# Performance work log

Hardware: AMD Instinct MI355X
Metric: run time of the kernel (lower is better)

## Reference

```python
import jax, jax.numpy as jnp
import numpy as np
from jax import lax

B, CIN, COUT, H, W = 4, 256, 256, 64, 64
K = 3  # kernel size
PAD = 1
STRIDE = 1


def setup_inputs() -> dict:
    key = jax.random.key(0)
    k1, k2, k3, k4 = jax.random.split(key, 4)
    x = jax.random.normal(k1, (B, CIN, H, W), dtype=jnp.float32)
    # small offset weights so learned offsets are modest (original init is zeros)
    offset_w = jax.random.normal(k2, (3 * K * K, CIN, K, K), dtype=jnp.float32) * 0.01
    offset_b = jax.random.normal(k3, (3 * K * K,), dtype=jnp.float32) * 0.01
    dcn_w = jax.random.normal(k4, (COUT, CIN, K, K), dtype=jnp.float32) * (1.0 / np.sqrt(CIN * K * K))
    return {"x": x, "offset_w": offset_w, "offset_b": offset_b, "dcn_w": dcn_w}


def _dcnv2(x, offset_w, offset_b, dcn_w):
    b, c, h, w = x.shape
    kk = K * K
    # offset conv (standard 3x3, stride 1, pad 1)
    o = lax.conv_general_dilated(
        x, offset_w, (STRIDE, STRIDE), ((PAD, PAD), (PAD, PAD)),
        dimension_numbers=("NCHW", "OIHW", "NCHW"))
    o = o + offset_b[None, :, None, None]
    ho, wo = o.shape[2], o.shape[3]
    off = o[:, : 2 * kk].reshape(b, kk, 2, ho, wo)  # pairs are (dy, dx)
    dy, dx = off[:, :, 0], off[:, :, 1]             # [b,kk,ho,wo]
    mask = jax.nn.sigmoid(o[:, 2 * kk:])            # [b,kk,ho,wo]

    ki, kj = jnp.meshgrid(jnp.arange(K), jnp.arange(K), indexing="ij")
    ki = ki.reshape(kk).astype(jnp.float32)
    kj = kj.reshape(kk).astype(jnp.float32)
    base_y = (jnp.arange(ho, dtype=jnp.float32) * STRIDE - PAD)[None, None, :, None] + ki[None, :, None, None]
    base_x = (jnp.arange(wo, dtype=jnp.float32) * STRIDE - PAD)[None, None, None, :] + kj[None, :, None, None]
    py = base_y + dy  # [b,kk,ho,wo] sampling y
    px = base_x + dx  # sampling x

    y0 = jnp.floor(py)
    x0 = jnp.floor(px)
    wy = py - y0  # bilinear fractional weights
    wx = px - x0
    y0i = y0.astype(jnp.int32)
    x0i = x0.astype(jnp.int32)

    xT = x.transpose(0, 2, 3, 1)  # [b,h,w,c] for channel-last gathers
    bidx = jnp.arange(b)[:, None, None, None]

    def gather(yi, xi):
        # zero padding outside the image
        valid = (yi >= 0) & (yi < h) & (xi >= 0) & (xi < w)
        yc = jnp.clip(yi, 0, h - 1)
        xc = jnp.clip(xi, 0, w - 1)
        v = xT[bidx, yc, xc]  # [b,kk,ho,wo,c]
        return v * valid[..., None].astype(x.dtype)

    g00 = gather(y0i, x0i)
    g01 = gather(y0i, x0i + 1)
    g10 = gather(y0i + 1, x0i)
    g11 = gather(y0i + 1, x0i + 1)

    wy_ = wy[..., None]
    wx_ = wx[..., None]
    sampled = (g00 * (1 - wy_) * (1 - wx_) + g01 * (1 - wy_) * wx_
               + g10 * wy_ * (1 - wx_) + g11 * wy_ * wx_)
    sampled = sampled * mask[..., None]  # modulation

    wk = dcn_w.reshape(dcn_w.shape[0], c, kk)  # [o,c,kk]
    return jnp.einsum("bkhwc,ock->bohw", sampled, wk)


def reference(x, offset_w, offset_b, dcn_w):
    return _dcnv2(x, offset_w, offset_b, dcn_w)
```

## Files before the change

### kernel.cpp

```cpp
#include <hip/hip_runtime.h>
#include <hip/hip_bf16.h>
#include <stdint.h>
#include <math.h>

#define KDIM 2304

typedef __attribute__((ext_vector_type(8))) short bf16x8;
typedef __attribute__((ext_vector_type(8))) unsigned short u16x8;
typedef __attribute__((ext_vector_type(4))) float f32x4;

__device__ inline unsigned short f2bf(float f) {
  union { float f; unsigned int u; } v; v.f = f;
  unsigned int u = v.u;
  unsigned int r = (u + 0x7FFFu + ((u >> 16) & 1u)) >> 16;
  return (unsigned short)r;
}
__device__ inline float bf2f(unsigned short h) {
  union { unsigned int u; float f; } v; v.u = ((unsigned int)h) << 16;
  return v.f;
}

__device__ inline void gl2lds16(const void* g, void* l) {
  __builtin_amdgcn_global_load_lds((const __attribute__((address_space(1))) void*)g,
                                   (__attribute__((address_space(3))) void*)l,
                                   16, 0, 0);
}

__global__ __launch_bounds__(256) void k_transpose(const float* __restrict__ x,
                                                   unsigned short* __restrict__ xTb) {
  __shared__ float tile[32][33];
  int t = threadIdx.x;
  int tx = t & 31, ty = t >> 5;
  int p0 = blockIdx.x * 32;
  int c0 = blockIdx.y * 32;
  int b  = blockIdx.z;
  const float* xb = x + ((size_t)b << 20);
#pragma unroll
  for (int i = 0; i < 4; ++i) {
    int c = c0 + ty + i * 8;
    tile[ty + i * 8][tx] = xb[((size_t)c << 12) + p0 + tx];
  }
  __syncthreads();
  unsigned short* ob = xTb + ((size_t)b << 20);
#pragma unroll
  for (int i = 0; i < 4; ++i) {
    int p = p0 + ty + i * 8;
    ob[(((size_t)p) << 8) + c0 + tx] = f2bf(tile[tx][ty + i * 8]);
  }
}

__global__ __launch_bounds__(256) void k_wprep(const float* __restrict__ dcn_w,
                                               const float* __restrict__ offset_w,
                                               unsigned short* __restrict__ Wpk,
                                               unsigned short* __restrict__ Wob,
                                               unsigned short* __restrict__ zp) {
  int gid = blockIdx.x * 256 + threadIdx.x;
  const int N1 = 72 * 8192;
  const int N2 = 32 * KDIM;
  if (gid < N1) {
    int j = gid & 7;
    int lane = (gid >> 3) & 63;
    int mb = (gid >> 9) & 15;
    int kc = gid >> 13;
    int row = mb * 16 + (lane & 15);
    int gk = kc * 32 + ((lane >> 4) << 3) + j;
    int c = gk & 255, kidx = gk >> 8;
    Wpk[gid] = f2bf(dcn_w[((size_t)(row * 256 + c)) * 9 + kidx]);
  } else if (gid < N1 + N2) {
    int g = gid - N1;
    int ch = g / KDIM, k = g % KDIM;
    int kidx = k >> 8, c = k & 255;
    Wob[g] = (ch < 27) ? f2bf(offset_w[((size_t)(ch * 256 + c)) * 9 + kidx])
                       : (unsigned short)0;
  } else if (gid < N1 + N2 + 128) {
    zp[gid - N1 - N2] = 0;
  }
}

__global__ __launch_bounds__(256) void k_offs_gemm(const unsigned short* __restrict__ xTb,
                                                   const unsigned short* __restrict__ Wob,
                                                   const unsigned short* __restrict__ zp,
                                                   const float* __restrict__ offb,
                                                   float* __restrict__ O2) {
  __shared__ unsigned short As[64 * 32];
  __shared__ unsigned short Bs[32 * 32];
  int t = threadIdx.x;
  int wv = t >> 6, lane = t & 63;
  int n0 = blockIdx.x * 64;
  int r0 = t >> 2, coff = (t & 3) * 8;

  int rowA = n0 + r0;
  int b_ = rowA >> 12, hw = rowA & 4095, h = hw >> 6, w = hw & 63;

  f32x4 acc[2] = {};
  char* AsB = (char*)As;
  char* BsB = (char*)Bs;

  for (int kt = 0; kt < 72; ++kt) {
    int k0 = kt * 32;
    int kidx = k0 >> 8, c0 = k0 & 255;
    int di = kidx / 3 - 1, dj = kidx % 3 - 1;
    {
      int y = h + di, xx = w + dj;
      const unsigned short* g = (y >= 0 && y < 64 && xx >= 0 && xx < 64)
          ? xTb + (((((size_t)b_) << 12) + (y << 6) + xx) << 8) + c0 + coff
          : zp;
      gl2lds16(g, AsB + wv * 1024);
    }
    if (t < 128) {
      const unsigned short* g = Wob + (size_t)(t >> 2) * KDIM + k0 + coff;
      gl2lds16(g, BsB + wv * 1024);
    }
    __syncthreads();
    bf16x8 aF, bF[2];
    aF = *(const bf16x8*)(As + (wv * 16 + (lane & 15)) * 32 + (lane >> 4) * 8);
#pragma unroll
    for (int j = 0; j < 2; ++j)
      bF[j] = *(const bf16x8*)(Bs + (j * 16 + (lane & 15)) * 32 + (lane >> 4) * 8);
#pragma unroll
    for (int j = 0; j < 2; ++j)
      acc[j] = __builtin_amdgcn_mfma_f32_16x16x32_bf16(aF, bF[j], acc[j], 0, 0, 0);
    __syncthreads();
  }

  int quad = lane >> 4, cl = lane & 15;
#pragma unroll
  for (int j = 0; j < 2; ++j) {
    int col = j * 16 + cl;
    float bias = (col < 27) ? offb[col] : 0.f;
#pragma unroll
    for (int r = 0; r < 4; ++r) {
      int row = n0 + wv * 16 + quad * 4 + r;
      O2[(size_t)row * 32 + col] = acc[j][r] + bias;
    }
  }
}

__global__ __launch_bounds__(256) void k_sweights(const float* __restrict__ O2,
                                                  float* __restrict__ SW) {
  int gid = blockIdx.x * 256 + threadIdx.x;
  if (gid >= 9 * 16384) return;
  int k = gid >> 14;
  int bhw = gid & 16383;
  int h = (bhw >> 6) & 63, w = bhw & 63;

  const float* o = O2 + (size_t)bhw * 32;
  float dy = o[2 * k];
  float dx = o[2 * k + 1];
  float mv = o[18 + k];
  float mask = 1.0f / (1.0f + expf(-mv));

  float py = (float)(h - 1 + k / 3) + dy;
  float px = (float)(w - 1 + k % 3) + dx;
  float y0f = floorf(py), x0f = floorf(px);
  float wy = py - y0f, wx = px - x0f;
  int y0 = (int)y0f, x0 = (int)x0f;
  int y1 = y0 + 1, x1 = x0 + 1;

  float vy0 = (y0 >= 0 && y0 < 64) ? 1.f : 0.f;
  float vy1 = (y1 >= 0 && y1 < 64) ? 1.f : 0.f;
  float vx0 = (x0 >= 0 && x0 < 64) ? 1.f : 0.f;
  float vx1 = (x1 >= 0 && x1 < 64) ? 1.f : 0.f;
  int y0c = min(max(y0, 0), 63), y1c = min(max(y1, 0), 63);
  int x0c = min(max(x0, 0), 63), x1c = min(max(x1, 0), 63);

  float4 wv4;
  wv4.x = (1.f - wy) * (1.f - wx) * vy0 * vx0 * mask;
  wv4.y = (1.f - wy) * wx * vy0 * vx1 * mask;
  wv4.z = wy * (1.f - wx) * vy1 * vx0 * mask;
  wv4.w = wy * wx * vy1 * vx1 * mask;
  uint4 ov;
  ov.x = (unsigned)(((y0c << 6) + x0c) << 8);
  ov.y = (unsigned)(((y0c << 6) + x1c) << 8);
  ov.z = (unsigned)(((y1c << 6) + x0c) << 8);
  ov.w = (unsigned)(((y1c << 6) + x1c) << 8);

  float* p = SW + (size_t)gid * 8;
  *(float4*)p = wv4;
  *(uint4*)(p + 4) = ov;
}

__global__ __launch_bounds__(256) void k_fused(const unsigned short* __restrict__ Wpk,
                                               const unsigned short* __restrict__ xTb,
                                               const float* __restrict__ SW,
                                               float* __restrict__ out) {
  __shared__ __align__(16) unsigned short Bs[2][64 * 40];
  int t = threadIdx.x;
  int wv = t >> 6, lane = t & 63;
  int n0 = blockIdx.x * 64;
  int b  = n0 >> 12;
  const unsigned short* xb = xTb + ((size_t)b << 20);

  int r = t >> 2, g = t & 3;
  int ch0 = g * 8;
  int bsw = r * 40 + ch0;

  const unsigned short* wpBase = Wpk + ((size_t)(wv * 4 * 64 + lane)) * 8;

  f32x4 acc[4][4] = {};

  float4 wv4; uint4 ov;
  {
    const float* sw = SW + ((size_t)(n0 + r)) * 8;
    wv4 = *(const float4*)sw;
    ov  = *(const uint4*)(sw + 4);
  }
  u16x8 q00, q01, q10, q11;
  bf16x8 aF[4], aFn[4];

  {
    int c = ch0;
    q00 = *(const u16x8*)(xb + ov.x + c);
    q01 = *(const u16x8*)(xb + ov.y + c);
    q10 = *(const u16x8*)(xb + ov.z + c);
    q11 = *(const u16x8*)(xb + ov.w + c);
#pragma unroll
    for (int i = 0; i < 4; ++i)
      aF[i] = *(const bf16x8*)(wpBase + (size_t)i * 512);
  }

#pragma unroll 2
  for (int kt = 0; kt < 72; ++kt) {
    float s[8];
#pragma unroll
    for (int c = 0; c < 8; ++c)
      s[c] = wv4.x * bf2f(q00[c]) + wv4.y * bf2f(q01[c])
           + wv4.z * bf2f(q10[c]) + wv4.w * bf2f(q11[c]);
    union { __hip_bfloat162 h2[4]; bf16x8 v; } pk;
#pragma unroll
    for (int c = 0; c < 4; ++c)
      pk.h2[c] = __float22bfloat162_rn(make_float2(s[2 * c], s[2 * c + 1]));
    *(bf16x8*)(&Bs[kt & 1][bsw]) = pk.v;

    if (kt < 71) {
      int kn = kt + 1;
      if ((kn & 7) == 0) {
        const float* sw = SW + ((size_t)(((kn >> 3) << 14) + n0 + r)) * 8;
        wv4 = *(const float4*)sw;
        ov  = *(const uint4*)(sw + 4);
      }
      int c = ((kn & 7) << 5) + ch0;
      q00 = *(const u16x8*)(xb + ov.x + c);
      q01 = *(const u16x8*)(xb + ov.y + c);
      q10 = *(const u16x8*)(xb + ov.z + c);
      q11 = *(const u16x8*)(xb + ov.w + c);
#pragma unroll
      for (int i = 0; i < 4; ++i)
        aFn[i] = *(const bf16x8*)(wpBase + ((size_t)kn * 16 + i) * 512);
    }

    __syncthreads();
    bf16x8 bF[4];
#pragma unroll
    for (int j = 0; j < 4; ++j)
      bF[j] = *(const bf16x8*)(&Bs[kt & 1][(j * 16 + (lane & 15)) * 40 + (lane >> 4) * 8]);
#pragma unroll
    for (int i = 0; i < 4; ++i)
#pragma unroll
      for (int j = 0; j < 4; ++j)
        acc[i][j] = __builtin_amdgcn_mfma_f32_16x16x32_bf16(aF[i], bF[j], acc[i][j], 0, 0, 0);
    if (kt < 71) {
#pragma unroll
      for (int i = 0; i < 4; ++i) aF[i] = aFn[i];
    }
  }

  int quad = lane >> 4, cl = lane & 15;
  float* ob = out + (((size_t)b) << 20);
#pragma unroll
  for (int i = 0; i < 4; ++i) {
    int mbase = wv * 64 + i * 16 + quad * 4;
#pragma unroll
    for (int j = 0; j < 4; ++j) {
      int hw = (n0 & 4095) + j * 16 + cl;
      float* op = ob + hw;
#pragma unroll
      for (int rr = 0; rr < 4; ++rr)
        op[((size_t)(mbase + rr)) << 12] = acc[i][j][rr];
    }
  }
}

extern "C" void kernel_launch(void* const* d_in, const int* in_sizes, int n_in,
                              void* d_out, int out_size, void* d_ws, size_t ws_size,
                              hipStream_t stream) {
  const float* x        = (const float*)d_in[0];
  const float* offset_w = (const float*)d_in[1];
  const float* offset_b = (const float*)d_in[2];
  const float* dcn_w    = (const float*)d_in[3];
  float* out = (float*)d_out;

  char* ws = (char*)d_ws;
  size_t off = 0;
  auto carve = [&](size_t bytes) -> void* {
    void* p = ws + off;
    off += (bytes + 255) & ~(size_t)255;
    return p;
  };
  unsigned short* xTb = (unsigned short*)carve(4ull * 64 * 64 * 256 * 2);
  unsigned short* Wpk = (unsigned short*)carve(72ull * 8192 * 2);
  unsigned short* Wob = (unsigned short*)carve(32ull * KDIM * 2);
  unsigned short* zp  = (unsigned short*)carve(256);
  float*          O2  = (float*)carve(16384ull * 32 * 4);
  float*          SW  = (float*)carve(9ull * 16384 * 8 * 4);
  (void)ws_size; (void)in_sizes; (void)n_in; (void)out_size;

  k_transpose<<<dim3(128, 8, 4), 256, 0, stream>>>(x, xTb);
  k_wprep<<<dim3((72 * 8192 + 32 * KDIM + 128 + 255) / 256), 256, 0, stream>>>(
      dcn_w, offset_w, Wpk, Wob, zp);
  k_offs_gemm<<<dim3(256), 256, 0, stream>>>(xTb, Wob, zp, offset_b, O2);
  k_sweights<<<dim3((9 * 16384 + 255) / 256), 256, 0, stream>>>(O2, SW);
  k_fused<<<dim3(256), 256, 0, stream>>>(Wpk, xTb, SW, out);
}
```

Baseline: 161.3 us.

## Split offset GEMM over K and widen fused kernel to eight waves

The offset-conv GEMM is split in half along K across a second grid dimension. The two partial results are summed together with the bias inside the sampling-weights kernel, which doubles the number of blocks for that small GEMM. The fused deformable GEMM now uses 512 threads with 8 waves split 4x2 over M and N. Each thread gathers and interpolates 4 channels instead of 8, and each wave holds half as many accumulators. The aim is more parallelism and latency hiding on 256 CUs, at the cost of extra partial-sum traffic and narrower gather loads.

```diff
diff --git a/kernel.cpp b/kernel.cpp
--- a/kernel.cpp
+++ b/kernel.cpp
@@ -6,7 +6,6 @@
 #define KDIM 2304
 
 typedef __attribute__((ext_vector_type(8))) short bf16x8;
-typedef __attribute__((ext_vector_type(8))) unsigned short u16x8;
 typedef __attribute__((ext_vector_type(4))) float f32x4;
 
 __device__ inline unsigned short f2bf(float f) {
@@ -80,13 +79,13 @@
 __global__ __launch_bounds__(256) void k_offs_gemm(const unsigned short* __restrict__ xTb,
                                                    const unsigned short* __restrict__ Wob,
                                                    const unsigned short* __restrict__ zp,
-                                                   const float* __restrict__ offb,
-                                                   float* __restrict__ O2) {
+                                                   float* __restrict__ O2p) {
   __shared__ unsigned short As[64 * 32];
   __shared__ unsigned short Bs[32 * 32];
   int t = threadIdx.x;
   int wv = t >> 6, lane = t & 63;
   int n0 = blockIdx.x * 64;
+  int z = blockIdx.y;
   int r0 = t >> 2, coff = (t & 3) * 8;
 
   int rowA = n0 + r0;
@@ -96,7 +95,7 @@
   char* AsB = (char*)As;
   char* BsB = (char*)Bs;
 
-  for (int kt = 0; kt < 72; ++kt) {
+  for (int kt = z * 36; kt < z * 36 + 36; ++kt) {
     int k0 = kt * 32;
     int kidx = k0 >> 8, c0 = k0 & 255;
     int di = kidx / 3 - 1, dj = kidx % 3 - 1;
@@ -124,19 +123,20 @@
   }
 
   int quad = lane >> 4, cl = lane & 15;
+  float* O2z = O2p + (size_t)z * 16384 * 32;
 #pragma unroll
   for (int j = 0; j < 2; ++j) {
     int col = j * 16 + cl;
-    float bias = (col < 27) ? offb[col] : 0.f;
 #pragma unroll
     for (int r = 0; r < 4; ++r) {
       int row = n0 + wv * 16 + quad * 4 + r;
-      O2[(size_t)row * 32 + col] = acc[j][r] + bias;
-    }
-  }
-}
-
-__global__ __launch_bounds__(256) void k_sweights(const float* __restrict__ O2,
+      O2z[(size_t)row * 32 + col] = acc[j][r];
+    }
+  }
+}
+
+__global__ __launch_bounds__(256) void k_sweights(const float* __restrict__ O2p,
+                                                  const float* __restrict__ offb,
                                                   float* __restrict__ SW) {
   int gid = blockIdx.x * 256 + threadIdx.x;
   if (gid >= 9 * 16384) return;
@@ -144,10 +144,11 @@
   int bhw = gid & 16383;
   int h = (bhw >> 6) & 63, w = bhw & 63;
 
-  const float* o = O2 + (size_t)bhw * 32;
-  float dy = o[2 * k];
-  float dx = o[2 * k + 1];
-  float mv = o[18 + k];
+  const float* o0 = O2p + (size_t)bhw * 32;
+  const float* o1 = o0 + (size_t)16384 * 32;
+  float dy = o0[2 * k]     + o1[2 * k]     + offb[2 * k];
+  float dx = o0[2 * k + 1] + o1[2 * k + 1] + offb[2 * k + 1];
+  float mv = o0[18 + k]    + o1[18 + k]    + offb[18 + k];
   float mask = 1.0f / (1.0f + expf(-mv));
 
   float py = (float)(h - 1 + k / 3) + dy;
@@ -180,24 +181,25 @@
   *(uint4*)(p + 4) = ov;
 }
 
-__global__ __launch_bounds__(256) void k_fused(const unsigned short* __restrict__ Wpk,
+__global__ __launch_bounds__(512) void k_fused(const unsigned short* __restrict__ Wpk,
                                                const unsigned short* __restrict__ xTb,
                                                const float* __restrict__ SW,
                                                float* __restrict__ out) {
   __shared__ __align__(16) unsigned short Bs[2][64 * 40];
   int t = threadIdx.x;
   int wv = t >> 6, lane = t & 63;
+  int wm = wv & 3, wn = wv >> 2;
   int n0 = blockIdx.x * 64;
   int b  = n0 >> 12;
   const unsigned short* xb = xTb + ((size_t)b << 20);
 
-  int r = t >> 2, g = t & 3;
-  int ch0 = g * 8;
+  int r = t >> 3, g = t & 7;
+  int ch0 = g * 4;
   int bsw = r * 40 + ch0;
 
-  const unsigned short* wpBase = Wpk + ((size_t)(wv * 4 * 64 + lane)) * 8;
-
-  f32x4 acc[4][4] = {};
+  const unsigned short* wpBase = Wpk + ((size_t)(wm * 4 * 64 + lane)) * 8;
+
+  f32x4 acc[4][2] = {};
 
   float4 wv4; uint4 ov;
   {
@@ -205,15 +207,15 @@
     wv4 = *(const float4*)sw;
     ov  = *(const uint4*)(sw + 4);
   }
-  u16x8 q00, q01, q10, q11;
+  ushort4 q00, q01, q10, q11;
   bf16x8 aF[4], aFn[4];
 
   {
-    int c = ch0;
-    q00 = *(const u16x8*)(xb + ov.x + c);
-    q01 = *(const u16x8*)(xb + ov.y + c);
-    q10 = *(const u16x8*)(xb + ov.z + c);
-    q11 = *(const u16x8*)(xb + ov.w + c);
+    unsigned c = (unsigned)ch0;
+    q00 = *(const ushort4*)(xb + ov.x + c);
+    q01 = *(const ushort4*)(xb + ov.y + c);
+    q10 = *(const ushort4*)(xb + ov.z + c);
+    q11 = *(const ushort4*)(xb + ov.w + c);
 #pragma unroll
     for (int i = 0; i < 4; ++i)
       aF[i] = *(const bf16x8*)(wpBase + (size_t)i * 512);
@@ -221,16 +223,15 @@
 
 #pragma unroll 2
   for (int kt = 0; kt < 72; ++kt) {
-    float s[8];
-#pragma unroll
-    for (int c = 0; c < 8; ++c)
-      s[c] = wv4.x * bf2f(q00[c]) + wv4.y * bf2f(q01[c])
-           + wv4.z * bf2f(q10[c]) + wv4.w * bf2f(q11[c]);
-    union { __hip_bfloat162 h2[4]; bf16x8 v; } pk;
-#pragma unroll
-    for (int c = 0; c < 4; ++c)
-      pk.h2[c] = __float22bfloat162_rn(make_float2(s[2 * c], s[2 * c + 1]));
-    *(bf16x8*)(&Bs[kt & 1][bsw]) = pk.v;
+    float s[4];
+    s[0] = wv4.x * bf2f(q00.x) + wv4.y * bf2f(q01.x) + wv4.z * bf2f(q10.x) + wv4.w * bf2f(q11.x);
+    s[1] = wv4.x * bf2f(q00.y) + wv4.y * bf2f(q01.y) + wv4.z * bf2f(q10.y) + wv4.w * bf2f(q11.y);
+    s[2] = wv4.x * bf2f(q00.z) + wv4.y * bf2f(q01.z) + wv4.z * bf2f(q10.z) + wv4.w * bf2f(q11.z);
+    s[3] = wv4.x * bf2f(q00.w) + wv4.y * bf2f(q01.w) + wv4.z * bf2f(q10.w) + wv4.w * bf2f(q11.w);
+    union { __hip_bfloat162 h2[2]; ushort4 v; } pk;
+    pk.h2[0] = __float22bfloat162_rn(make_float2(s[0], s[1]));
+    pk.h2[1] = __float22bfloat162_rn(make_float2(s[2], s[3]));
+    *(ushort4*)(&Bs[kt & 1][bsw]) = pk.v;
 
     if (kt < 71) {
       int kn = kt + 1;
@@ -239,25 +240,25 @@
         wv4 = *(const float4*)sw;
         ov  = *(const uint4*)(sw + 4);
       }
-      int c = ((kn & 7) << 5) + ch0;
-      q00 = *(const u16x8*)(xb + ov.x + c);
-      q01 = *(const u16x8*)(xb + ov.y + c);
-      q10 = *(const u16x8*)(xb + ov.z + c);
-      q11 = *(const u16x8*)(xb + ov.w + c);
+      unsigned c = (unsigned)(((kn & 7) << 5) + ch0);
+      q00 = *(const ushort4*)(xb + ov.x + c);
+      q01 = *(const ushort4*)(xb + ov.y + c);
+      q10 = *(const ushort4*)(xb + ov.z + c);
+      q11 = *(const ushort4*)(xb + ov.w + c);
 #pragma unroll
       for (int i = 0; i < 4; ++i)
         aFn[i] = *(const bf16x8*)(wpBase + ((size_t)kn * 16 + i) * 512);
     }
 
     __syncthreads();
-    bf16x8 bF[4];
-#pragma unroll
-    for (int j = 0; j < 4; ++j)
-      bF[j] = *(const bf16x8*)(&Bs[kt & 1][(j * 16 + (lane & 15)) * 40 + (lane >> 4) * 8]);
+    bf16x8 bF[2];
+#pragma unroll
+    for (int j = 0; j < 2; ++j)
+      bF[j] = *(const bf16x8*)(&Bs[kt & 1][(wn * 32 + j * 16 + (lane & 15)) * 40 + (lane >> 4) * 8]);
 #pragma unroll
     for (int i = 0; i < 4; ++i)
 #pragma unroll
-      for (int j = 0; j < 4; ++j)
+      for (int j = 0; j < 2; ++j)
         acc[i][j] = __builtin_amdgcn_mfma_f32_16x16x32_bf16(aF[i], bF[j], acc[i][j], 0, 0, 0);
     if (kt < 71) {
 #pragma unroll
@@ -269,10 +270,10 @@
   float* ob = out + (((size_t)b) << 20);
 #pragma unroll
   for (int i = 0; i < 4; ++i) {
-    int mbase = wv * 64 + i * 16 + quad * 4;
-#pragma unroll
-    for (int j = 0; j < 4; ++j) {
-      int hw = (n0 & 4095) + j * 16 + cl;
+    int mbase = wm * 64 + i * 16 + quad * 4;
+#pragma unroll
+    for (int j = 0; j < 2; ++j) {
+      int hw = (n0 & 4095) + wn * 32 + j * 16 + cl;
       float* op = ob + hw;
 #pragma unroll
       for (int rr = 0; rr < 4; ++rr)
@@ -301,14 +302,14 @@
   unsigned short* Wpk = (unsigned short*)carve(72ull * 8192 * 2);
   unsigned short* Wob = (unsigned short*)carve(32ull * KDIM * 2);
   unsigned short* zp  = (unsigned short*)carve(256);
-  float*          O2  = (float*)carve(16384ull * 32 * 4);
+  float*          O2p = (float*)carve(2ull * 16384 * 32 * 4);
   float*          SW  = (float*)carve(9ull * 16384 * 8 * 4);
   (void)ws_size; (void)in_sizes; (void)n_in; (void)out_size;
 
   k_transpose<<<dim3(128, 8, 4), 256, 0, stream>>>(x, xTb);
   k_wprep<<<dim3((72 * 8192 + 32 * KDIM + 128 + 255) / 256), 256, 0, stream>>>(
       dcn_w, offset_w, Wpk, Wob, zp);
-  k_offs_gemm<<<dim3(256), 256, 0, stream>>>(xTb, Wob, zp, offset_b, O2);
-  k_sweights<<<dim3((9 * 16384 + 255) / 256), 256, 0, stream>>>(O2, SW);
-  k_fused<<<dim3(256), 256, 0, stream>>>(Wpk, xTb, SW, out);
-}
+  k_offs_gemm<<<dim3(256, 2), 256, 0, stream>>>(xTb, Wob, zp, O2p);
+  k_sweights<<<dim3((9 * 16384 + 255) / 256), 256, 0, stream>>>(O2p, offset_b, SW);
+  k_fused<<<dim3(256), 512, 0, stream>>>(Wpk, xTb, SW, out);
+}
```

After: 153.4 us. -4.9%, faster.

## Drop LDS staging in offset and fused GEMMs, load operands directly into registers

Applied to the files above, without the earlier changes.

The offset-conv GEMM now loads A and B fragments straight from global memory into registers with software prefetch, replacing the global_load_lds staging and its block barriers. The bias add moves into the sampling-weights kernel. The fused deformable GEMM now uses 512 threads per block, and each wave computes its own bilinear-sampled B fragments in registers, so the LDS buffer and per-iteration __syncthreads are gone. The cost is that each sampled column is no longer shared across waves through LDS: each of the four M-waves repeats the gather and interpolation for its columns, and register pressure goes up.

```diff
diff --git a/kernel.cpp b/kernel.cpp
--- a/kernel.cpp
+++ b/kernel.cpp
@@ -18,12 +18,6 @@
 __device__ inline float bf2f(unsigned short h) {
   union { unsigned int u; float f; } v; v.u = ((unsigned int)h) << 16;
   return v.f;
-}
-
-__device__ inline void gl2lds16(const void* g, void* l) {
-  __builtin_amdgcn_global_load_lds((const __attribute__((address_space(1))) void*)g,
-                                   (__attribute__((address_space(3))) void*)l,
-                                   16, 0, 0);
 }
 
 __global__ __launch_bounds__(256) void k_transpose(const float* __restrict__ x,
@@ -72,7 +66,7 @@
     int kidx = k >> 8, c = k & 255;
     Wob[g] = (ch < 27) ? f2bf(offset_w[((size_t)(ch * 256 + c)) * 9 + kidx])
                        : (unsigned short)0;
-  } else if (gid < N1 + N2 + 128) {
+  } else if (gid < N1 + N2 + 256) {
     zp[gid - N1 - N2] = 0;
   }
 }
@@ -80,63 +74,58 @@
 __global__ __launch_bounds__(256) void k_offs_gemm(const unsigned short* __restrict__ xTb,
                                                    const unsigned short* __restrict__ Wob,
                                                    const unsigned short* __restrict__ zp,
-                                                   const float* __restrict__ offb,
                                                    float* __restrict__ O2) {
-  __shared__ unsigned short As[64 * 32];
-  __shared__ unsigned short Bs[32 * 32];
   int t = threadIdx.x;
   int wv = t >> 6, lane = t & 63;
-  int n0 = blockIdx.x * 64;
-  int r0 = t >> 2, coff = (t & 3) * 8;
-
-  int rowA = n0 + r0;
-  int b_ = rowA >> 12, hw = rowA & 4095, h = hw >> 6, w = hw & 63;
+  int cl = lane & 15, q = lane >> 4;
+  int rowbase = (blockIdx.x * 4 + wv) * 16;
+  int row = rowbase + cl;
+  int b_ = row >> 12, hw = row & 4095, h = hw >> 6, w = hw & 63;
+  const unsigned short* xbb = xTb + (((size_t)b_) << 20);
+
+  const unsigned short* pB0 = Wob + (size_t)cl * KDIM + q * 8;
+  const unsigned short* pB1 = Wob + (size_t)(16 + cl) * KDIM + q * 8;
 
   f32x4 acc[2] = {};
-  char* AsB = (char*)As;
-  char* BsB = (char*)Bs;
-
+
+  auto aptr = [&](int kidx) -> const unsigned short* {
+    int di = kidx / 3 - 1, dj = kidx % 3 - 1;
+    int y = h + di, xx = w + dj;
+    bool v = ((unsigned)y < 64u) && ((unsigned)xx < 64u);
+    return v ? xbb + (((size_t)((y << 6) + xx)) << 8) + q * 8 : zp + q * 8;
+  };
+
+  const unsigned short* pA = aptr(0);
+  bf16x8 aC = *(const bf16x8*)pA;
+  bf16x8 b0C = *(const bf16x8*)pB0;
+  bf16x8 b1C = *(const bf16x8*)pB1;
+
+#pragma unroll 2
   for (int kt = 0; kt < 72; ++kt) {
-    int k0 = kt * 32;
-    int kidx = k0 >> 8, c0 = k0 & 255;
-    int di = kidx / 3 - 1, dj = kidx % 3 - 1;
-    {
-      int y = h + di, xx = w + dj;
-      const unsigned short* g = (y >= 0 && y < 64 && xx >= 0 && xx < 64)
-          ? xTb + (((((size_t)b_) << 12) + (y << 6) + xx) << 8) + c0 + coff
-          : zp;
-      gl2lds16(g, AsB + wv * 1024);
-    }
-    if (t < 128) {
-      const unsigned short* g = Wob + (size_t)(t >> 2) * KDIM + k0 + coff;
-      gl2lds16(g, BsB + wv * 1024);
-    }
-    __syncthreads();
-    bf16x8 aF, bF[2];
-    aF = *(const bf16x8*)(As + (wv * 16 + (lane & 15)) * 32 + (lane >> 4) * 8);
-#pragma unroll
-    for (int j = 0; j < 2; ++j)
-      bF[j] = *(const bf16x8*)(Bs + (j * 16 + (lane & 15)) * 32 + (lane >> 4) * 8);
-#pragma unroll
-    for (int j = 0; j < 2; ++j)
-      acc[j] = __builtin_amdgcn_mfma_f32_16x16x32_bf16(aF, bF[j], acc[j], 0, 0, 0);
-    __syncthreads();
-  }
-
-  int quad = lane >> 4, cl = lane & 15;
-#pragma unroll
-  for (int j = 0; j < 2; ++j) {
-    int col = j * 16 + cl;
-    float bias = (col < 27) ? offb[col] : 0.f;
+    bf16x8 aN, b0N, b1N;
+    if (kt < 71) {
+      int kn = kt + 1;
+      if ((kn & 7) == 0) pA = aptr(kn >> 3);
+      aN  = *(const bf16x8*)(pA + (kn & 7) * 32);
+      b0N = *(const bf16x8*)(pB0 + kn * 32);
+      b1N = *(const bf16x8*)(pB1 + kn * 32);
+    }
+    acc[0] = __builtin_amdgcn_mfma_f32_16x16x32_bf16(aC, b0C, acc[0], 0, 0, 0);
+    acc[1] = __builtin_amdgcn_mfma_f32_16x16x32_bf16(aC, b1C, acc[1], 0, 0, 0);
+    if (kt < 71) { aC = aN; b0C = b0N; b1C = b1N; }
+  }
+
+#pragma unroll
+  for (int j = 0; j < 2; ++j)
 #pragma unroll
     for (int r = 0; r < 4; ++r) {
-      int row = n0 + wv * 16 + quad * 4 + r;
-      O2[(size_t)row * 32 + col] = acc[j][r] + bias;
-    }
-  }
+      int orow = rowbase + q * 4 + r;
+      O2[(size_t)orow * 32 + j * 16 + cl] = acc[j][r];
+    }
 }
 
 __global__ __launch_bounds__(256) void k_sweights(const float* __restrict__ O2,
+                                                  const float* __restrict__ offb,
                                                   float* __restrict__ SW) {
   int gid = blockIdx.x * 256 + threadIdx.x;
   if (gid >= 9 * 16384) return;
@@ -145,9 +134,9 @@
   int h = (bhw >> 6) & 63, w = bhw & 63;
 
   const float* o = O2 + (size_t)bhw * 32;
-  float dy = o[2 * k];
-  float dx = o[2 * k + 1];
-  float mv = o[18 + k];
+  float dy = o[2 * k]     + offb[2 * k];
+  float dx = o[2 * k + 1] + offb[2 * k + 1];
+  float mv = o[18 + k]    + offb[18 + k];
   float mask = 1.0f / (1.0f + expf(-mv));
 
   float py = (float)(h - 1 + k / 3) + dy;
@@ -180,103 +169,116 @@
   *(uint4*)(p + 4) = ov;
 }
 
-__global__ __launch_bounds__(256) void k_fused(const unsigned short* __restrict__ Wpk,
+__global__ __launch_bounds__(512) void k_fused(const unsigned short* __restrict__ Wpk,
                                                const unsigned short* __restrict__ xTb,
                                                const float* __restrict__ SW,
                                                float* __restrict__ out) {
-  __shared__ __align__(16) unsigned short Bs[2][64 * 40];
   int t = threadIdx.x;
   int wv = t >> 6, lane = t & 63;
-  int n0 = blockIdx.x * 64;
-  int b  = n0 >> 12;
+  int wm = wv & 3, wn = wv >> 2;
+  int cl = lane & 15, q = lane >> 4;
+  int nb = blockIdx.x;
+  int n0 = nb * 64 + wn * 32;
+  int b  = (nb * 64) >> 12;
   const unsigned short* xb = xTb + ((size_t)b << 20);
 
-  int r = t >> 2, g = t & 3;
-  int ch0 = g * 8;
-  int bsw = r * 40 + ch0;
-
-  const unsigned short* wpBase = Wpk + ((size_t)(wv * 4 * 64 + lane)) * 8;
-
-  f32x4 acc[4][4] = {};
-
-  float4 wv4; uint4 ov;
+  int r0 = n0 + cl;
+  int r1 = n0 + 16 + cl;
+
+  const unsigned short* wpBase = Wpk + ((size_t)(wm * 4 * 64 + lane)) * 8;
+
+  f32x4 acc[4][2] = {};
+
+  float4 wq0, wq1; uint4 ov0, ov1;
   {
-    const float* sw = SW + ((size_t)(n0 + r)) * 8;
-    wv4 = *(const float4*)sw;
-    ov  = *(const uint4*)(sw + 4);
-  }
-  u16x8 q00, q01, q10, q11;
-  bf16x8 aF[4], aFn[4];
-
-  {
-    int c = ch0;
-    q00 = *(const u16x8*)(xb + ov.x + c);
-    q01 = *(const u16x8*)(xb + ov.y + c);
-    q10 = *(const u16x8*)(xb + ov.z + c);
-    q11 = *(const u16x8*)(xb + ov.w + c);
-#pragma unroll
-    for (int i = 0; i < 4; ++i)
-      aF[i] = *(const bf16x8*)(wpBase + (size_t)i * 512);
-  }
-
-#pragma unroll 2
+    const float* s0 = SW + ((size_t)r0) * 8;
+    const float* s1 = SW + ((size_t)r1) * 8;
+    wq0 = *(const float4*)s0; ov0 = *(const uint4*)(s0 + 4);
+    wq1 = *(const float4*)s1; ov1 = *(const uint4*)(s1 + 4);
+  }
+
+  int qo = q * 8;
+  u16x8 c00, c01, c02, c03;
+  u16x8 c10, c11, c12, c13;
+  bf16x8 aF[4];
+
+  c00 = *(const u16x8*)(xb + ov0.x + qo); c01 = *(const u16x8*)(xb + ov0.y + qo);
+  c02 = *(const u16x8*)(xb + ov0.z + qo); c03 = *(const u16x8*)(xb + ov0.w + qo);
+  c10 = *(const u16x8*)(xb + ov1.x + qo); c11 = *(const u16x8*)(xb + ov1.y + qo);
+  c12 = *(const u16x8*)(xb + ov1.z + qo); c13 = *(const u16x8*)(xb + ov1.w + qo);
+#pragma unroll
+  for (int i = 0; i < 4; ++i)
+    aF[i] = *(const bf16x8*)(wpBase + (size_t)i * 512);
+
   for (int kt = 0; kt < 72; ++kt) {
-    float s[8];
-#pragma unroll
-    for (int c = 0; c < 8; ++c)
-      s[c] = wv4.x * bf2f(q00[c]) + wv4.y * bf2f(q01[c])
-           + wv4.z * bf2f(q10[c]) + wv4.w * bf2f(q11[c]);
-    union { __hip_bfloat162 h2[4]; bf16x8 v; } pk;
-#pragma unroll
-    for (int c = 0; c < 4; ++c)
-      pk.h2[c] = __float22bfloat162_rn(make_float2(s[2 * c], s[2 * c + 1]));
-    *(bf16x8*)(&Bs[kt & 1][bsw]) = pk.v;
-
+    bf16x8 bF0, bF1;
+    {
+      float s[8];
+#pragma unroll
+      for (int c = 0; c < 8; ++c)
+        s[c] = wq0.x * bf2f(c00[c]) + wq0.y * bf2f(c01[c])
+             + wq0.z * bf2f(c02[c]) + wq0.w * bf2f(c03[c]);
+      union { __hip_bfloat162 h2[4]; bf16x8 v; } pk;
+#pragma unroll
+      for (int c = 0; c < 4; ++c)
+        pk.h2[c] = __float22bfloat162_rn(make_float2(s[2 * c], s[2 * c + 1]));
+      bF0 = pk.v;
+    }
+    {
+      float s[8];
+#pragma unroll
+      for (int c = 0; c < 8; ++c)
+        s[c] = wq1.x * bf2f(c10[c]) + wq1.y * bf2f(c11[c])
+             + wq1.z * bf2f(c12[c]) + wq1.w * bf2f(c13[c]);
+      union { __hip_bfloat162 h2[4]; bf16x8 v; } pk;
+#pragma unroll
+      for (int c = 0; c < 4; ++c)
+        pk.h2[c] = __float22bfloat162_rn(make_float2(s[2 * c], s[2 * c + 1]));
+      bF1 = pk.v;
+    }
+
+    bf16x8 aN[4];
     if (kt < 71) {
       int kn = kt + 1;
       if ((kn & 7) == 0) {
-        const float* sw = SW + ((size_t)(((kn >> 3) << 14) + n0 + r)) * 8;
-        wv4 = *(const float4*)sw;
-        ov  = *(const uint4*)(sw + 4);
+        int kidx = kn >> 3;
+        const float* s0 = SW + ((size_t)((kidx << 14) + r0)) * 8;
+        const float* s1 = SW + ((size_t)((kidx << 14) + r1)) * 8;
+        wq0 = *(const float4*)s0; ov0 = *(const uint4*)(s0 + 4);
+        wq1 = *(const float4*)s1; ov1 = *(const uint4*)(s1 + 4);
       }
-      int c = ((kn & 7) << 5) + ch0;
-      q00 = *(const u16x8*)(xb + ov.x + c);
-      q01 = *(const u16x8*)(xb + ov.y + c);
-      q10 = *(const u16x8*)(xb + ov.z + c);
-      q11 = *(const u16x8*)(xb + ov.w + c);
+      unsigned co = (unsigned)(((kn & 7) << 5) + qo);
+      c00 = *(const u16x8*)(xb + ov0.x + co); c01 = *(const u16x8*)(xb + ov0.y + co);
+      c02 = *(const u16x8*)(xb + ov0.z + co); c03 = *(const u16x8*)(xb + ov0.w + co);
+      c10 = *(const u16x8*)(xb + ov1.x + co); c11 = *(const u16x8*)(xb + ov1.y + co);
+      c12 = *(const u16x8*)(xb + ov1.z + co); c13 = *(const u16x8*)(xb + ov1.w + co);
 #pragma unroll
       for (int i = 0; i < 4; ++i)
-        aFn[i] = *(const bf16x8*)(wpBase + ((size_t)kn * 16 + i) * 512);
-    }
-
-    __syncthreads();
-    bf16x8 bF[4];
-#pragma unroll
-    for (int j = 0; j < 4; ++j)
-      bF[j] = *(const bf16x8*)(&Bs[kt & 1][(j * 16 + (lane & 15)) * 40 + (lane >> 4) * 8]);
-#pragma unroll
-    for (int i = 0; i < 4; ++i)
-#pragma unroll
-      for (int j = 0; j < 4; ++j)
-        acc[i][j] = __builtin_amdgcn_mfma_f32_16x16x32_bf16(aF[i], bF[j], acc[i][j], 0, 0, 0);
+        aN[i] = *(const bf16x8*)(wpBase + ((size_t)kn * 16 + i) * 512);
+    }
+
+#pragma unroll
+    for (int i = 0; i < 4; ++i) {
+      acc[i][0] = __builtin_amdgcn_mfma_f32_16x16x32_bf16(aF[i], bF0, acc[i][0], 0, 0, 0);
+      acc[i][1] = __builtin_amdgcn_mfma_f32_16x16x32_bf16(aF[i], bF1, acc[i][1], 0, 0, 0);
+    }
     if (kt < 71) {
 #pragma unroll
-      for (int i = 0; i < 4; ++i) aF[i] = aFn[i];
-    }
-  }
-
-  int quad = lane >> 4, cl = lane & 15;
+      for (int i = 0; i < 4; ++i) aF[i] = aN[i];
+    }
+  }
+
   float* ob = out + (((size_t)b) << 20);
+  int hwb = (n0 & 4095);
 #pragma unroll
   for (int i = 0; i < 4; ++i) {
-    int mbase = wv * 64 + i * 16 + quad * 4;
-#pragma unroll
-    for (int j = 0; j < 4; ++j) {
-      int hw = (n0 & 4095) + j * 16 + cl;
-      float* op = ob + hw;
-#pragma unroll
-      for (int rr = 0; rr < 4; ++rr)
-        op[((size_t)(mbase + rr)) << 12] = acc[i][j][rr];
+    int mbase = wm * 64 + i * 16 + q * 4;
+#pragma unroll
+    for (int j = 0; j < 2; ++j) {
+      float* op = ob + hwb + j * 16 + cl;
+#pragma unroll
+      for (int r = 0; r < 4; ++r)
+        op[((size_t)(mbase + r)) << 12] = acc[i][j][r];
     }
   }
 }
@@ -300,15 +302,15 @@
   unsigned short* xTb = (unsigned short*)carve(4ull * 64 * 64 * 256 * 2);
   unsigned short* Wpk = (unsigned short*)carve(72ull * 8192 * 2);
   unsigned short* Wob = (unsigned short*)carve(32ull * KDIM * 2);
-  unsigned short* zp  = (unsigned short*)carve(256);
+  unsigned short* zp  = (unsigned short*)carve(512);
   float*          O2  = (float*)carve(16384ull * 32 * 4);
   float*          SW  = (float*)carve(9ull * 16384 * 8 * 4);
   (void)ws_size; (void)in_sizes; (void)n_in; (void)out_size;
 
   k_transpose<<<dim3(128, 8, 4), 256, 0, stream>>>(x, xTb);
-  k_wprep<<<dim3((72 * 8192 + 32 * KDIM + 128 + 255) / 256), 256, 0, stream>>>(
+  k_wprep<<<dim3((72 * 8192 + 32 * KDIM + 256 + 255) / 256), 256, 0, stream>>>(
       dcn_w, offset_w, Wpk, Wob, zp);
-  k_offs_gemm<<<dim3(256), 256, 0, stream>>>(xTb, Wob, zp, offset_b, O2);
-  k_sweights<<<dim3((9 * 16384 + 255) / 256), 256, 0, stream>>>(O2, SW);
-  k_fused<<<dim3(256), 256, 0, stream>>>(Wpk, xTb, SW, out);
-}
+  k_offs_gemm<<<dim3(256), 256, 0, stream>>>(xTb, Wob, zp, O2);
+  k_sweights<<<dim3((9 * 16384 + 255) / 256), 256, 0, stream>>>(O2, offset_b, SW);
+  k_fused<<<dim3(256), 512, 0, stream>>>(Wpk, xTb, SW, out);
+}
```

Result: slower. 248.0 us (+53.7%).
